# Kernel tuning notes

Hardware: AMD Instinct MI355X
Metric: run time of the kernel (lower is better)

The kernel has to match this reference:

```python
import jax, jax.numpy as jnp
import numpy as np

B, S = 2, 2048
HID = 2560
NH, NKV, HD = 20, 5, 128
GROUPS = NH // NKV  # 4
THETA = 500000.0
RMS_EPS = 1e-6  # RMSNorm default eps used for attn_sub_norm
NEG_INF = -1e9


def pack_ternary(key, M, K):
    """Pack ternary weights {-1,0,1} (stored as trits {0,1,2}) into SIMD
    block-interleaved uint8 layout: per 128-elem block, byte j holds
    weights j+0 (bits 6:7), j+32 (4:5), j+64 (2:3), j+96 (0:1)."""
    t = jax.random.randint(key, (M, K), 0, 3).astype(jnp.uint8)
    t = t.reshape(M, K // 128, 4, 32)
    byte = (t[:, :, 0] << 6) | (t[:, :, 1] << 4) | (t[:, :, 2] << 2) | t[:, :, 3]
    return byte.reshape(M, K // 4)


def unpack_ternary(packed):
    """Inverse of pack_ternary -> float weights in {-1,0,1}. (M, K//4) -> (M, K)."""
    M, Kp = packed.shape
    nb = Kp // 32
    b = packed.reshape(M, nb, 32)
    fields = jnp.stack([(b >> 6) & 3, (b >> 4) & 3, (b >> 2) & 3, b & 3], axis=2)
    return fields.reshape(M, nb * 128).astype(jnp.float32) - 1.0


def bitlinear(x, packed, scale):
    w = unpack_ternary(packed) * scale  # (out, in)
    return jnp.einsum('bsi,oi->bso', x, w)


def rotate_half(x):
    h = x.shape[-1] // 2
    return jnp.concatenate([-x[..., h:], x[..., :h]], axis=-1)


def rms_norm(x, w, eps=RMS_EPS):
    var = jnp.mean(jnp.square(x.astype(jnp.float32)), axis=-1, keepdims=True)
    return (w * (x * jax.lax.rsqrt(var + eps))).astype(x.dtype)


def setup_inputs() -> dict:
    key = jax.random.key(0)
    ks = jax.random.split(key, 6)
    hidden_states = jax.random.normal(ks[0], (B, S, HID), dtype=jnp.float32)
    causal = jnp.tril(jnp.ones((S, S), dtype=bool))
    attention_mask = jnp.where(causal, 0.0, NEG_INF).astype(jnp.float32)[None, None]
    return {
        'hidden_states': hidden_states,
        'attention_mask': attention_mask,
        'q_w': pack_ternary(ks[1], NH * HD, HID),
        'k_w': pack_ternary(ks[2], NKV * HD, HID),
        'v_w': pack_ternary(ks[3], NKV * HD, HID),
        'o_w': pack_ternary(ks[4], HID, NH * HD),
        'q_scale': jnp.float32(0.02),
        'k_scale': jnp.float32(0.02),
        'v_scale': jnp.float32(0.02),
        'o_scale': jnp.float32(0.02),
        'attn_norm_w': jnp.ones((NH * HD,), dtype=jnp.float32),
    }


def reference(hidden_states, attention_mask, q_w, k_w, v_w, o_w,
              q_scale, k_scale, v_scale, o_scale, attn_norm_w):
    bsz, seq_len, _ = hidden_states.shape
    q = bitlinear(hidden_states, q_w, q_scale)
    k = bitlinear(hidden_states, k_w, k_scale)
    v = bitlinear(hidden_states, v_w, v_scale)
    q = q.reshape(bsz, seq_len, NH, HD).transpose(0, 2, 1, 3)    # (b,h,s,d)
    k = k.reshape(bsz, seq_len, NKV, HD).transpose(0, 2, 1, 3)
    v = v.reshape(bsz, seq_len, NKV, HD).transpose(0, 2, 1, 3)
    # rotary embedding
    inv_freq = 1.0 / (THETA ** (jnp.arange(0, HD, 2, dtype=jnp.float32) / HD))
    t = jnp.arange(seq_len, dtype=jnp.float32)
    freqs = t[:, None] * inv_freq[None, :]            # (s, d/2)
    emb = jnp.concatenate([freqs, freqs], axis=-1)    # (s, d)
    cos, sin = jnp.cos(emb), jnp.sin(emb)
    q = q * cos + rotate_half(q) * sin
    k = k * cos + rotate_half(k) * sin
    # GQA: repeat kv heads
    k = jnp.repeat(k, GROUPS, axis=1)
    v = jnp.repeat(v, GROUPS, axis=1)
    scores = jnp.einsum('bhqd,bhkd->bhqk', q, k) / np.sqrt(HD).astype(np.float32)
    scores = scores + attention_mask
    attn = jax.nn.softmax(scores.astype(jnp.float32), axis=-1).astype(q.dtype)
    out = jnp.einsum('bhqk,bhkd->bhqd', attn, v)
    out = out.transpose(0, 2, 1, 3).reshape(bsz, seq_len, NH * HD)
    out = rms_norm(out, attn_norm_w)
    return bitlinear(out, o_w, o_scale)
```

## Files before the change

kernel.cpp:

```cpp
#include <hip/hip_runtime.h>
#include <cstdint>
#include <cstddef>

typedef __bf16 bf16x8 __attribute__((ext_vector_type(8)));
typedef float  f32x4  __attribute__((ext_vector_type(4)));
typedef int    i32x4  __attribute__((ext_vector_type(4)));
typedef unsigned short u16x4 __attribute__((ext_vector_type(4)));

#define DEV __device__ __forceinline__
#define NEGINF (-__builtin_inff())

DEV uint16_t f2bf(float f) {
  union { float f; uint32_t u; } v; v.f = f;
  uint32_t u = v.u;
  u += 0x7FFFu + ((u >> 16) & 1u);
  return (uint16_t)(u >> 16);
}
DEV float bf2f(uint16_t h) {
  union { uint32_t u; float f; } v; v.u = ((uint32_t)h) << 16;
  return v.f;
}

DEV void gload_lds16(const void* g, void* l) {
  __builtin_amdgcn_global_load_lds(
      (const __attribute__((address_space(1))) void*)g,
      (__attribute__((address_space(3))) void*)l, 16, 0, 0);
}


__global__ void k_prep(const float* __restrict__ x, uint16_t* __restrict__ xb,
                       const uint32_t* __restrict__ qw, const uint32_t* __restrict__ kw,
                       const uint32_t* __restrict__ vw, const uint32_t* __restrict__ ow,
                       uint16_t* __restrict__ wqkv, uint16_t* __restrict__ owb,
                       const float* __restrict__ g,
                       float* __restrict__ cosT, float* __restrict__ sinT)
{
  const int bid = blockIdx.x, tid = threadIdx.x;
  if (bid < 10240) {
    const int i = bid * 256 + tid;
    f32x4 v = *(const f32x4*)(x + (size_t)i * 4);
    u16x4 o;
    o[0] = f2bf(v[0]); o[1] = f2bf(v[1]); o[2] = f2bf(v[2]); o[3] = f2bf(v[3]);
    *(u16x4*)(xb + (size_t)i * 4) = o;
  } else if (bid < 26240) {
    const int idx = (bid - 10240) * 256 + tid;
    if (idx < 2457600) {
      int local = (idx < 1638400) ? idx : ((idx < 2048000) ? idx - 1638400 : idx - 2048000);
      const uint32_t* s = (idx < 1638400) ? qw : ((idx < 2048000) ? kw : vw);
      uint32_t b = s[local] & 0xFFu;
      int drow = idx / 640, pc = idx - drow * 640;
      int blk = pc >> 5, j = pc & 31;
      size_t base = (size_t)drow * 2560 + (size_t)blk * 128 + j;
      wqkv[base]      = f2bf((float)((b >> 6) & 3u) - 1.0f);
      wqkv[base + 32] = f2bf((float)((b >> 4) & 3u) - 1.0f);
      wqkv[base + 64] = f2bf((float)((b >> 2) & 3u) - 1.0f);
      wqkv[base + 96] = f2bf((float)(b & 3u) - 1.0f);
    } else {
      int local = idx - 2457600;
      uint32_t b = ow[local] & 0xFFu;
      int drow = local / 640, pc = local - drow * 640;
      int blk = pc >> 5, j = pc & 31;
      int kpos = blk * 128 + j;
      size_t base = (size_t)drow * 2560 + kpos;
      owb[base]      = f2bf(((float)((b >> 6) & 3u) - 1.0f) * g[kpos]);
      owb[base + 32] = f2bf(((float)((b >> 4) & 3u) - 1.0f) * g[kpos + 32]);
      owb[base + 64] = f2bf(((float)((b >> 2) & 3u) - 1.0f) * g[kpos + 64]);
      owb[base + 96] = f2bf(((float)(b & 3u) - 1.0f) * g[kpos + 96]);
    }
  } else {
    const int idx = (bid - 26240) * 256 + tid;
    const int s = idx >> 6, i = idx & 63;
    float inv = expf((float)i * (-13.122363377404328f / 64.0f));
    float fr = (float)s * inv;
    cosT[idx] = cosf(fr);
    sinT[idx] = sinf(fr);
  }
}

__global__ void k_rope(uint16_t* __restrict__ buf, const float* __restrict__ cosT,
                       const float* __restrict__ sinT, int H, int total,
                       float* __restrict__ ss)
{
  int idx = blockIdx.x * blockDim.x + threadIdx.x;
  if (blockIdx.x < 16) ss[blockIdx.x * 256 + threadIdx.x] = 0.f;
  if (idx >= total) return;
  int d = idx & 63;
  int t = idx >> 6;
  int h = t % H;
  int row = t / H;
  int s = row & 2047;
  size_t base = (size_t)row * (size_t)(H * 128) + (size_t)h * 128 + d;
  float x1 = bf2f(buf[base]), x2 = bf2f(buf[base + 64]);
  float c = cosT[(s << 6) + d], sn = sinT[(s << 6) + d];
  buf[base]      = f2bf(x1 * c - x2 * sn);
  buf[base + 64] = f2bf(x2 * c + x1 * sn);
}

template<int MODE>
__global__ __launch_bounds__(256, 2)
void k_gemm(const uint16_t* __restrict__ A, const uint16_t* __restrict__ W,
            uint16_t* __restrict__ Qo, uint16_t* __restrict__ Ko, uint16_t* __restrict__ Vo,
            float* __restrict__ Fo,
            const float* __restrict__ s0p, const float* __restrict__ s1p, const float* __restrict__ s2p,
            int M, int N, int K)
{
  __shared__ uint16_t As[128 * 64];
  __shared__ uint16_t Bs[128 * 64];
  const int tid = threadIdx.x;
  const int n0 = blockIdx.x * 128, m0 = blockIdx.y * 128;
  const int lane = tid & 63, w = tid >> 6;
  const int wm = (w >> 1) * 64, wn = (w & 1) * 64;
  const int lr = lane & 15, lg = lane >> 4, lk = lg * 8;
  const size_t K2 = (size_t)K * 2;
  f32x4 acc[4][4] = {};

  const int srow = tid >> 3;
  const int cprime = ((tid & 7) * 16) ^ ((srow & 7) << 4);
  const uint8_t* Ag = (const uint8_t*)A + (size_t)(m0 + srow) * K2 + cprime;
  const uint8_t* Wg = (const uint8_t*)W + (size_t)(n0 + srow) * K2 + cprime;
  char* Al = (char*)As + w * 1024;
  char* Bl = (char*)Bs + w * 1024;

  for (size_t k0b = 0; k0b < K2; k0b += 128) {
    #pragma unroll
    for (int i = 0; i < 4; ++i)
      gload_lds16(Ag + (size_t)(i * 32) * K2 + k0b, Al + i * 4096);
    #pragma unroll
    for (int i = 0; i < 4; ++i)
      gload_lds16(Wg + (size_t)(i * 32) * K2 + k0b, Bl + i * 4096);
    __syncthreads();
    #pragma unroll
    for (int kc = 0; kc < 64; kc += 32) {
      bf16x8 a[4], b[4];
      #pragma unroll
      for (int i = 0; i < 4; ++i) {
        const int r = wm + i * 16 + lr;
        a[i] = *(const bf16x8*)((const char*)As + r * 128 + (((kc + lk) * 2) ^ ((r & 7) << 4)));
      }
      #pragma unroll
      for (int j = 0; j < 4; ++j) {
        const int r = wn + j * 16 + lr;
        b[j] = *(const bf16x8*)((const char*)Bs + r * 128 + (((kc + lk) * 2) ^ ((r & 7) << 4)));
      }
      #pragma unroll
      for (int i = 0; i < 4; ++i)
        #pragma unroll
        for (int j = 0; j < 4; ++j)
          acc[i][j] = __builtin_amdgcn_mfma_f32_16x16x32_bf16(a[i], b[j], acc[i][j], 0, 0, 0);
    }
    __syncthreads();
  }

  if (MODE == 0) {
    const float qs = *s0p, ks = *s1p, vs = *s2p;
    #pragma unroll
    for (int i = 0; i < 4; ++i) {
      const int rowb = m0 + wm + i * 16 + lg * 4;
      #pragma unroll
      for (int j = 0; j < 4; ++j) {
        const int col = n0 + wn + j * 16 + lr;
        #pragma unroll
        for (int r = 0; r < 4; ++r) {
          const int rr = rowb + r;
          const float v = acc[i][j][r];
          if (col < 2560) {
            Qo[(size_t)rr * 2560 + col] = f2bf(v * qs);
          } else if (col < 3200) {
            Ko[(size_t)rr * 640 + (col - 2560)] = f2bf(v * ks);
          } else {
            const int n2 = col - 3200;
            const int kvh = n2 >> 7, d = n2 & 127;
            const int bb = rr >> 11, ss2 = rr & 2047;
            Vo[(((size_t)(bb * 5 + kvh) * 128 + d) << 11) + ss2] = f2bf(v * vs);
          }
        }
      }
    }
  } else {
    const float os = *s0p;
    #pragma unroll
    for (int i = 0; i < 4; ++i) {
      const int rowb = m0 + wm + i * 16 + lg * 4;
      #pragma unroll
      for (int j = 0; j < 4; ++j) {
        const int col = n0 + wn + j * 16 + lr;
        #pragma unroll
        for (int r = 0; r < 4; ++r) {
          const float rs = rsqrtf(s1p[rowb + r] * (1.0f / 2560.0f) + 1e-6f);
          Fo[(size_t)(rowb + r) * N + col] = acc[i][j][r] * os * rs;
        }
      }
    }
  }
}

__global__ __launch_bounds__(256, 2)
void k_attn(const uint16_t* __restrict__ Q, const uint16_t* __restrict__ Kb,
            const uint16_t* __restrict__ Vt, uint16_t* __restrict__ Ob,
            const float* __restrict__ cosT, const float* __restrict__ sinT,
            float* __restrict__ ssb)
{
  __shared__ char Klds[2][16384];
  __shared__ char Vlds[2][16384];
  __shared__ uint16_t p_lds[4][16][72];

  const int lin = blockIdx.x;
  const int gslot = (lin & 7) * 80 + (lin >> 3);
  const int bk = gslot >> 6;
  const int st = 63 - (gslot & 63);
  const int b = bk / 5, kvh = bk - b * 5;

  const int tid = threadIdx.x, lane = tid & 63, w = tid >> 6;
  const int lr = lane & 15, lg = lane >> 4, lk = lg * 8;
  const int h = kvh * 4 + w;
  uint16_t (*pl)[72] = p_lds[w];
  const int kswz = (lr & 7) << 4;

  const uint8_t* Kg = (const uint8_t*)(Kb + (size_t)b * 2048 * 640 + (size_t)kvh * 128);
  const uint8_t* Vg = (const uint8_t*)(Vt + ((size_t)(b * 5 + kvh) * 128) * 2048);

  const int krow = tid >> 4;
  const int kcol = ((tid & 15) * 16) ^ ((krow & 7) << 4);
  const int vrow = tid >> 3;
  const int vcol = ((tid & 7) * 16) ^ ((vrow & 7) << 4);
  const int dst16 = tid * 16;

  const float C = 0.127531019577f;

  const int q0 = st * 32;
  const int ns = (q0 + 95) >> 6;

  bf16x8 qf0[4], qf1[4];
  {
    const size_t qb0 = ((size_t)(b * 2048 + q0 + lr)) * 2560 + (size_t)h * 128 + lk;
    #pragma unroll
    for (int c = 0; c < 4; ++c) {
      qf0[c] = *(const bf16x8*)&Q[qb0 + c * 32];
      qf1[c] = *(const bf16x8*)&Q[qb0 + 16 * 2560 + c * 32];
    }
  }
  #pragma unroll
  for (int g = 0; g < 2; ++g) {
    bf16x8* qf = g ? qf1 : qf0;
    const int s = q0 + 16 * g + lr;
    const int tb0 = s * 64 + lg * 8;
    #pragma unroll
    for (int c = 0; c < 2; ++c) {
      const int tb = tb0 + c * 32;
      f32x4 csa = *(const f32x4*)&cosT[tb];
      f32x4 csb = *(const f32x4*)&cosT[tb + 4];
      f32x4 sna = *(const f32x4*)&sinT[tb];
      f32x4 snb = *(const f32x4*)&sinT[tb + 4];
      #pragma unroll
      for (int j = 0; j < 8; ++j) {
        const float cs = (j < 4) ? csa[j] : csb[j - 4];
        const float sn = (j < 4) ? sna[j] : snb[j - 4];
        const float x1 = (float)qf[c][j], x2 = (float)qf[c + 2][j];
        qf[c][j]     = (__bf16)(x1 * cs - x2 * sn);
        qf[c + 2][j] = (__bf16)(x2 * cs + x1 * sn);
      }
    }
  }

  {
    const uint8_t* Ks = Kg + (size_t)krow * 1280 + kcol;
    const uint8_t* Vs = Vg + (size_t)vrow * 4096 + vcol;
    #pragma unroll
    for (int i = 0; i < 4; ++i) gload_lds16(Ks + (size_t)i * 16 * 1280, Klds[0] + dst16 + i * 4096);
    #pragma unroll
    for (int i = 0; i < 4; ++i) gload_lds16(Vs + (size_t)i * 32 * 4096, Vlds[0] + dst16 + i * 4096);
  }

  int cur = 0;
  float m0 = NEGINF, m1 = NEGINF, l0 = 0.f, l1 = 0.f;
  f32x4 oa0[8] = {}, oa1[8] = {};

  #pragma unroll 1
  for (int stp = 0; stp < ns; ++stp) {
    const int k0 = stp * 64;
    __syncthreads();

    if (stp + 1 < ns) {
      const int kn = k0 + 64;
      const uint8_t* Ks = Kg + (size_t)(kn + krow) * 1280 + kcol;
      const uint8_t* Vs = Vg + (size_t)vrow * 4096 + (size_t)kn * 2 + vcol;
      char* Kd = Klds[cur ^ 1] + dst16;
      char* Vd = Vlds[cur ^ 1] + dst16;
      #pragma unroll
      for (int i = 0; i < 4; ++i) gload_lds16(Ks + (size_t)i * 16 * 1280, Kd + i * 4096);
      #pragma unroll
      for (int i = 0; i < 4; ++i) gload_lds16(Vs + (size_t)i * 32 * 4096, Vd + i * 4096);
    }

    const char* Kc = Klds[cur];
    const char* Vc = Vlds[cur];

    __builtin_amdgcn_s_setprio(1);
    f32x4 sa0[4] = {}, sa1[4] = {};
    #pragma unroll
    for (int t = 0; t < 4; ++t) {
      #pragma unroll
      for (int c = 0; c < 4; ++c) {
        bf16x8 kf = *(const bf16x8*)(Kc + (t * 16 + lr) * 256 + ((c * 64 + lg * 16) ^ kswz));
        sa0[t] = __builtin_amdgcn_mfma_f32_16x16x32_bf16(kf, qf0[c], sa0[t], 0, 0, 0);
        sa1[t] = __builtin_amdgcn_mfma_f32_16x16x32_bf16(kf, qf1[c], sa1[t], 0, 0, 0);
      }
    }
    __builtin_amdgcn_s_setprio(0);

    #pragma unroll
    for (int g = 0; g < 2; ++g) {
      const f32x4* sa = g ? sa1 : sa0;
      f32x4* oa = g ? oa1 : oa0;
      float& m = g ? m1 : m0;
      float& l = g ? l1 : l0;
      const int q0g = q0 + 16 * g;

      float sraw[16];
      if (k0 + 63 > q0g) {
        #pragma unroll
        for (int t = 0; t < 4; ++t)
          #pragma unroll
          for (int r = 0; r < 4; ++r)
            sraw[t * 4 + r] = (k0 + t * 16 + lg * 4 + r <= q0g + lr) ? sa[t][r] : NEGINF;
      } else {
        #pragma unroll
        for (int t = 0; t < 4; ++t)
          #pragma unroll
          for (int r = 0; r < 4; ++r)
            sraw[t * 4 + r] = sa[t][r];
      }
      float a01 = fmaxf(sraw[0], sraw[1]),   a23 = fmaxf(sraw[2], sraw[3]);
      float a45 = fmaxf(sraw[4], sraw[5]),   a67 = fmaxf(sraw[6], sraw[7]);
      float a89 = fmaxf(sraw[8], sraw[9]),   aab = fmaxf(sraw[10], sraw[11]);
      float acd = fmaxf(sraw[12], sraw[13]), aef = fmaxf(sraw[14], sraw[15]);
      float mxr = fmaxf(fmaxf(fmaxf(a01, a23), fmaxf(a45, a67)),
                        fmaxf(fmaxf(a89, aab), fmaxf(acd, aef)));
      mxr = fmaxf(mxr, __shfl_xor(mxr, 16));
      mxr = fmaxf(mxr, __shfl_xor(mxr, 32));
      const float mx_u = mxr * C;
      if (!__all(mx_u <= m + 8.0f)) {
        const float mn = fmaxf(m, mx_u);
        const float resc = __builtin_exp2f(m - mn);
        m = mn;
        l *= resc;
        #pragma unroll
        for (int dc = 0; dc < 8; ++dc) {
          oa[dc][0] *= resc; oa[dc][1] *= resc; oa[dc][2] *= resc; oa[dc][3] *= resc;
        }
      }
      const float nm = -m;
      float pv[16];
      #pragma unroll
      for (int i = 0; i < 16; ++i) pv[i] = __builtin_exp2f(fmaf(sraw[i], C, nm));
      float s0 = (pv[0] + pv[1]) + (pv[2] + pv[3]);
      float s1 = (pv[4] + pv[5]) + (pv[6] + pv[7]);
      float s2 = (pv[8] + pv[9]) + (pv[10] + pv[11]);
      float s3 = (pv[12] + pv[13]) + (pv[14] + pv[15]);
      l += (s0 + s1) + (s2 + s3);
      #pragma unroll
      for (int t = 0; t < 4; ++t) {
        union { __bf16 b4[4]; unsigned long long u64; } pk;
        #pragma unroll
        for (int r = 0; r < 4; ++r) pk.b4[r] = (__bf16)pv[t * 4 + r];
        *(unsigned long long*)&pl[lr][t * 16 + lg * 4] = pk.u64;
      }
      bf16x8 pa0 = *(const bf16x8*)&pl[lr][lk];
      bf16x8 pa1 = *(const bf16x8*)&pl[lr][32 + lk];
      __builtin_amdgcn_s_setprio(1);
      #pragma unroll
      for (int dc = 0; dc < 8; ++dc) {
        bf16x8 vf0 = *(const bf16x8*)(Vc + (dc * 16 + lr) * 128 + ((lg * 16) ^ kswz));
        bf16x8 vf1 = *(const bf16x8*)(Vc + (dc * 16 + lr) * 128 + ((64 + lg * 16) ^ kswz));
        oa[dc] = __builtin_amdgcn_mfma_f32_16x16x32_bf16(vf0, pa0, oa[dc], 0, 0, 0);
        oa[dc] = __builtin_amdgcn_mfma_f32_16x16x32_bf16(vf1, pa1, oa[dc], 0, 0, 0);
      }
      __builtin_amdgcn_s_setprio(0);
    }
    cur ^= 1;
  }

  #pragma unroll
  for (int g = 0; g < 2; ++g) {
    f32x4* oa = g ? oa1 : oa0;
    float lf = g ? l1 : l0;
    lf += __shfl_xor(lf, 16);
    lf += __shfl_xor(lf, 32);
    const float inv = 1.0f / lf;
    const size_t obase = ((size_t)(b * 2048 + q0 + 16 * g + lr)) * 2560 + (size_t)h * 128;
    float ssq = 0.f;
    #pragma unroll
    for (int dc = 0; dc < 8; ++dc) {
      union { __bf16 b4[4]; unsigned long long u64; } ok;
      #pragma unroll
      for (int r = 0; r < 4; ++r) {
        ok.b4[r] = (__bf16)(oa[dc][r] * inv);
        const float vq = (float)ok.b4[r];
        ssq += vq * vq;
      }
      *(unsigned long long*)&Ob[obase + dc * 16 + lg * 4] = ok.u64;
    }
    ssq += __shfl_xor(ssq, 16);
    ssq += __shfl_xor(ssq, 32);
    if (lane < 16)
      atomicAdd(&ssb[b * 2048 + q0 + 16 * g + lr], ssq);
  }
}

extern "C" void kernel_launch(void* const* d_in, const int* in_sizes, int n_in,
                              void* d_out, int out_size, void* d_ws, size_t ws_size,
                              hipStream_t stream)
{
  const float*    x     = (const float*)d_in[0];
  const uint32_t* qw    = (const uint32_t*)d_in[2];
  const uint32_t* kw    = (const uint32_t*)d_in[3];
  const uint32_t* vw    = (const uint32_t*)d_in[4];
  const uint32_t* ow    = (const uint32_t*)d_in[5];
  const float*    qs    = (const float*)d_in[6];
  const float*    ks    = (const float*)d_in[7];
  const float*    vs    = (const float*)d_in[8];
  const float*    os    = (const float*)d_in[9];
  const float*    gnorm = (const float*)d_in[10];

  char* ws = (char*)d_ws;
  uint16_t* xb   = (uint16_t*)(ws + 0);
  uint16_t* wqkv = (uint16_t*)(ws + 20971520);
  uint16_t* owb  = (uint16_t*)(ws + 40632320);
  float*    cosT = (float*)   (ws + 53739520);
  float*    sinT = (float*)   (ws + 54263808);
  uint16_t* Qb   = (uint16_t*)(ws + 54788096);
  uint16_t* Kb   = (uint16_t*)(ws + 75759616);
  uint16_t* Vt   = (uint16_t*)(ws + 81002496);
  float*    ssb  = (float*)   (ws + 20971520);

  k_prep<<<26752, 256, 0, stream>>>(x, xb, qw, kw, vw, ow, wqkv, owb, gnorm, cosT, sinT);

  k_gemm<0><<<dim3(30, 32), 256, 0, stream>>>(xb, wqkv, Qb, Kb, Vt, nullptr,
                                              qs, ks, vs, 4096, 3840, 2560);
  k_rope<<<5120, 256, 0, stream>>>(Kb, cosT, sinT, 5, 1310720, ssb);

  k_attn<<<dim3(640), 256, 0, stream>>>(Qb, Kb, Vt, xb, cosT, sinT, ssb);

  k_gemm<1><<<dim3(20, 32), 256, 0, stream>>>(xb, owb, nullptr, nullptr, nullptr,
                                              (float*)d_out, os, ssb, nullptr,
                                              4096, 2560, 2560);
}
```

Before: 287.8 us.

## Fuse K rotary embedding into QKV GEMM epilogue and drop atomic sum-of-squares

Removes the separate k_rope kernel by applying rotary embedding to K inside the QKV GEMM epilogue, staging the K tile in LDS so each element can read its rotate-half partner. The attention kernel now reduces its per-row sum of squares across the four waves in LDS and writes one partial per KV head instead of using atomicAdd. The output GEMM sums the five partials before computing the RMS scale. This saves a kernel launch, a read-modify-write pass over K, and the zeroing and atomics for the norm buffer, at the cost of an extra LDS round trip and barrier in the K-column GEMM blocks.

```diff
diff --git a/kernel.cpp b/kernel.cpp
--- a/kernel.cpp
+++ b/kernel.cpp
@@ -77,35 +77,16 @@
   }
 }
 
-__global__ void k_rope(uint16_t* __restrict__ buf, const float* __restrict__ cosT,
-                       const float* __restrict__ sinT, int H, int total,
-                       float* __restrict__ ss)
-{
-  int idx = blockIdx.x * blockDim.x + threadIdx.x;
-  if (blockIdx.x < 16) ss[blockIdx.x * 256 + threadIdx.x] = 0.f;
-  if (idx >= total) return;
-  int d = idx & 63;
-  int t = idx >> 6;
-  int h = t % H;
-  int row = t / H;
-  int s = row & 2047;
-  size_t base = (size_t)row * (size_t)(H * 128) + (size_t)h * 128 + d;
-  float x1 = bf2f(buf[base]), x2 = bf2f(buf[base + 64]);
-  float c = cosT[(s << 6) + d], sn = sinT[(s << 6) + d];
-  buf[base]      = f2bf(x1 * c - x2 * sn);
-  buf[base + 64] = f2bf(x2 * c + x1 * sn);
-}
-
 template<int MODE>
 __global__ __launch_bounds__(256, 2)
 void k_gemm(const uint16_t* __restrict__ A, const uint16_t* __restrict__ W,
             uint16_t* __restrict__ Qo, uint16_t* __restrict__ Ko, uint16_t* __restrict__ Vo,
             float* __restrict__ Fo,
             const float* __restrict__ s0p, const float* __restrict__ s1p, const float* __restrict__ s2p,
+            const float* __restrict__ cosT, const float* __restrict__ sinT,
             int M, int N, int K)
 {
-  __shared__ uint16_t As[128 * 64];
-  __shared__ uint16_t Bs[128 * 64];
+  __shared__ uint16_t smem[2][128 * 64];
   const int tid = threadIdx.x;
   const int n0 = blockIdx.x * 128, m0 = blockIdx.y * 128;
   const int lane = tid & 63, w = tid >> 6;
@@ -118,8 +99,8 @@
   const int cprime = ((tid & 7) * 16) ^ ((srow & 7) << 4);
   const uint8_t* Ag = (const uint8_t*)A + (size_t)(m0 + srow) * K2 + cprime;
   const uint8_t* Wg = (const uint8_t*)W + (size_t)(n0 + srow) * K2 + cprime;
-  char* Al = (char*)As + w * 1024;
-  char* Bl = (char*)Bs + w * 1024;
+  char* Al = (char*)smem[0] + w * 1024;
+  char* Bl = (char*)smem[1] + w * 1024;
 
   for (size_t k0b = 0; k0b < K2; k0b += 128) {
     #pragma unroll
@@ -135,12 +116,12 @@
       #pragma unroll
       for (int i = 0; i < 4; ++i) {
         const int r = wm + i * 16 + lr;
-        a[i] = *(const bf16x8*)((const char*)As + r * 128 + (((kc + lk) * 2) ^ ((r & 7) << 4)));
+        a[i] = *(const bf16x8*)((const char*)smem[0] + r * 128 + (((kc + lk) * 2) ^ ((r & 7) << 4)));
       }
       #pragma unroll
       for (int j = 0; j < 4; ++j) {
         const int r = wn + j * 16 + lr;
-        b[j] = *(const bf16x8*)((const char*)Bs + r * 128 + (((kc + lk) * 2) ^ ((r & 7) << 4)));
+        b[j] = *(const bf16x8*)((const char*)smem[1] + r * 128 + (((kc + lk) * 2) ^ ((r & 7) << 4)));
       }
       #pragma unroll
       for (int i = 0; i < 4; ++i)
@@ -152,43 +133,85 @@
   }
 
   if (MODE == 0) {
-    const float qs = *s0p, ks = *s1p, vs = *s2p;
+    if (n0 >= 2560 && n0 < 3200) {
+      const float ks = *s1p;
+      uint16_t* Kx = (uint16_t*)smem;
+      #pragma unroll
+      for (int i = 0; i < 4; ++i) {
+        const int rowl = wm + i * 16 + lg * 4;
+        #pragma unroll
+        for (int j = 0; j < 4; ++j) {
+          const int coll = wn + j * 16 + lr;
+          #pragma unroll
+          for (int r = 0; r < 4; ++r)
+            Kx[(rowl + r) * 128 + coll] = f2bf(acc[i][j][r] * ks);
+        }
+      }
+      __syncthreads();
+      const int ncol = n0 - 2560;
+      #pragma unroll
+      for (int i = 0; i < 4; ++i) {
+        const int rowl = wm + i * 16 + lg * 4;
+        #pragma unroll
+        for (int j = 0; j < 4; ++j) {
+          const int coll = wn + j * 16 + lr;
+          const int d = coll & 63;
+          #pragma unroll
+          for (int r = 0; r < 4; ++r) {
+            const int rr = m0 + rowl + r;
+            const int spos = rr & 2047;
+            const float xv = bf2f(Kx[(rowl + r) * 128 + coll]);
+            const float pv = bf2f(Kx[(rowl + r) * 128 + (coll ^ 64)]);
+            const float cs = cosT[spos * 64 + d];
+            const float sn = sinT[spos * 64 + d];
+            const float out = (coll < 64) ? (xv * cs - pv * sn) : (xv * cs + pv * sn);
+            Ko[(size_t)rr * 640 + ncol + coll] = f2bf(out);
+          }
+        }
+      }
+    } else {
+      const float qs = *s0p, vs = *s2p;
+      #pragma unroll
+      for (int i = 0; i < 4; ++i) {
+        const int rowb = m0 + wm + i * 16 + lg * 4;
+        #pragma unroll
+        for (int j = 0; j < 4; ++j) {
+          const int col = n0 + wn + j * 16 + lr;
+          #pragma unroll
+          for (int r = 0; r < 4; ++r) {
+            const int rr = rowb + r;
+            const float v = acc[i][j][r];
+            if (col < 2560) {
+              Qo[(size_t)rr * 2560 + col] = f2bf(v * qs);
+            } else {
+              const int n2 = col - 3200;
+              const int kvh = n2 >> 7, d = n2 & 127;
+              const int bb = rr >> 11, ss2 = rr & 2047;
+              Vo[(((size_t)(bb * 5 + kvh) * 128 + d) << 11) + ss2] = f2bf(v * vs);
+            }
+          }
+        }
+      }
+    }
+  } else {
+    const float os = *s0p;
     #pragma unroll
     for (int i = 0; i < 4; ++i) {
       const int rowb = m0 + wm + i * 16 + lg * 4;
+      float rs4[4];
+      #pragma unroll
+      for (int r = 0; r < 4; ++r) {
+        const int row = rowb + r;
+        const float tot = s1p[row] + s1p[4096 + row] + s1p[8192 + row] +
+                          s1p[12288 + row] + s1p[16384 + row];
+        rs4[r] = rsqrtf(tot * (1.0f / 2560.0f) + 1e-6f) * os;
+      }
       #pragma unroll
       for (int j = 0; j < 4; ++j) {
         const int col = n0 + wn + j * 16 + lr;
         #pragma unroll
-        for (int r = 0; r < 4; ++r) {
-          const int rr = rowb + r;
-          const float v = acc[i][j][r];
-          if (col < 2560) {
-            Qo[(size_t)rr * 2560 + col] = f2bf(v * qs);
-          } else if (col < 3200) {
-            Ko[(size_t)rr * 640 + (col - 2560)] = f2bf(v * ks);
-          } else {
-            const int n2 = col - 3200;
-            const int kvh = n2 >> 7, d = n2 & 127;
-            const int bb = rr >> 11, ss2 = rr & 2047;
-            Vo[(((size_t)(bb * 5 + kvh) * 128 + d) << 11) + ss2] = f2bf(v * vs);
-          }
-        }
-      }
-    }
-  } else {
-    const float os = *s0p;
-    #pragma unroll
-    for (int i = 0; i < 4; ++i) {
-      const int rowb = m0 + wm + i * 16 + lg * 4;
-      #pragma unroll
-      for (int j = 0; j < 4; ++j) {
-        const int col = n0 + wn + j * 16 + lr;
-        #pragma unroll
-        for (int r = 0; r < 4; ++r) {
-          const float rs = rsqrtf(s1p[rowb + r] * (1.0f / 2560.0f) + 1e-6f);
-          Fo[(size_t)(rowb + r) * N + col] = acc[i][j][r] * os * rs;
-        }
+        for (int r = 0; r < 4; ++r)
+          Fo[(size_t)(rowb + r) * N + col] = acc[i][j][r] * rs4[r];
       }
     }
   }
@@ -198,11 +221,12 @@
 void k_attn(const uint16_t* __restrict__ Q, const uint16_t* __restrict__ Kb,
             const uint16_t* __restrict__ Vt, uint16_t* __restrict__ Ob,
             const float* __restrict__ cosT, const float* __restrict__ sinT,
-            float* __restrict__ ssb)
+            float* __restrict__ pss)
 {
   __shared__ char Klds[2][16384];
   __shared__ char Vlds[2][16384];
   __shared__ uint16_t p_lds[4][16][72];
+  __shared__ float xss[4][32];
 
   const int lin = blockIdx.x;
   const int gslot = (lin & 7) * 80 + (lin >> 3);
@@ -380,6 +404,7 @@
     cur ^= 1;
   }
 
+  float ssqg[2];
   #pragma unroll
   for (int g = 0; g < 2; ++g) {
     f32x4* oa = g ? oa1 : oa0;
@@ -402,8 +427,13 @@
     }
     ssq += __shfl_xor(ssq, 16);
     ssq += __shfl_xor(ssq, 32);
-    if (lane < 16)
-      atomicAdd(&ssb[b * 2048 + q0 + 16 * g + lr], ssq);
+    ssqg[g] = ssq;
+  }
+  if (lane < 16) { xss[w][lr] = ssqg[0]; xss[w][16 + lr] = ssqg[1]; }
+  __syncthreads();
+  if (tid < 32) {
+    const float tot = xss[0][tid] + xss[1][tid] + xss[2][tid] + xss[3][tid];
+    pss[kvh * 4096 + b * 2048 + q0 + tid] = tot;
   }
 }
 
@@ -431,17 +461,16 @@
   uint16_t* Qb   = (uint16_t*)(ws + 54788096);
   uint16_t* Kb   = (uint16_t*)(ws + 75759616);
   uint16_t* Vt   = (uint16_t*)(ws + 81002496);
-  float*    ssb  = (float*)   (ws + 20971520);
+  float*    pss  = (float*)   (ws + 20971520);
 
   k_prep<<<26752, 256, 0, stream>>>(x, xb, qw, kw, vw, ow, wqkv, owb, gnorm, cosT, sinT);
 
   k_gemm<0><<<dim3(30, 32), 256, 0, stream>>>(xb, wqkv, Qb, Kb, Vt, nullptr,
-                                              qs, ks, vs, 4096, 3840, 2560);
-  k_rope<<<5120, 256, 0, stream>>>(Kb, cosT, sinT, 5, 1310720, ssb);
-
-  k_attn<<<dim3(640), 256, 0, stream>>>(Qb, Kb, Vt, xb, cosT, sinT, ssb);
+                                              qs, ks, vs, cosT, sinT, 4096, 3840, 2560);
+
+  k_attn<<<dim3(640), 256, 0, stream>>>(Qb, Kb, Vt, xb, cosT, sinT, pss);
 
   k_gemm<1><<<dim3(20, 32), 256, 0, stream>>>(xb, owb, nullptr, nullptr, nullptr,
-                                              (float*)d_out, os, ssb, nullptr,
+                                              (float*)d_out, os, pss, nullptr, cosT, sinT,
                                               4096, 2560, 2560);
 }
```

Result: no change. 284.9 us (median of 2 runs) (-1.0%).
